# Kernel tuning notes

Measured on AMD Instinct MI355X. Metric: run time of the kernel, lower is better.

## Reference

```python
import jax, jax.numpy as jnp
import numpy as np

DIM = 4096
N_HEADS = 32
HEAD_DIM = 128
N_KV_HEADS = 8
KV_REPEATS = N_HEADS // N_KV_HEADS
SLIDING_WINDOW = 4096
SEQLEN = 2048
SCALE = HEAD_DIM ** -0.5
NEG = -1e9


def calculate_rope(x, cos, sin):
    # x: [S, H, D]; cos/sin: [S, D//2] applied to interleaved channel pairs
    x1, x2 = x[..., ::2], x[..., 1::2]
    c, s = cos[:, None, :], sin[:, None, :]
    r1 = x1 * c - x2 * s
    r2 = x1 * s + x2 * c
    return jnp.stack([r1, r2], axis=-1).reshape(x.shape)


def setup_inputs() -> dict:
    key = jax.random.key(0)
    ks = jax.random.split(key, 8)
    x = jax.random.normal(ks[0], (SEQLEN, DIM), dtype=jnp.float32)
    # rotary tables
    inv_freq = 1.0 / (10000.0 ** (np.arange(0, HEAD_DIM, 2, dtype=np.float32) / HEAD_DIM))
    t = np.arange(SEQLEN, dtype=np.float32)
    freqs = np.outer(t, inv_freq)  # [S, D/2]
    cos_freq = jnp.asarray(np.cos(freqs), dtype=jnp.float32)
    sin_freq = jnp.asarray(np.sin(freqs), dtype=jnp.float32)
    positions = jnp.arange(SEQLEN, dtype=jnp.int32)
    # causal sliding-window additive mask
    i = np.arange(SEQLEN)[:, None]
    j = np.arange(SEQLEN)[None, :]
    allow = (j <= i) & (j > i - SLIDING_WINDOW)
    mask = jnp.asarray(np.where(allow, 0.0, NEG), dtype=jnp.float32)
    cache_k = jnp.zeros((SLIDING_WINDOW, N_KV_HEADS, HEAD_DIM), dtype=jnp.float32)
    cache_v = jnp.zeros((SLIDING_WINDOW, N_KV_HEADS, HEAD_DIM), dtype=jnp.float32)
    # eqx.nn.Linear weights have shape (out_features, in_features)
    sd = DIM ** -0.5
    wq = jax.random.normal(ks[1], (N_HEADS * HEAD_DIM, DIM), dtype=jnp.float32) * sd
    wk = jax.random.normal(ks[2], (N_KV_HEADS * HEAD_DIM, DIM), dtype=jnp.float32) * sd
    wv = jax.random.normal(ks[3], (N_KV_HEADS * HEAD_DIM, DIM), dtype=jnp.float32) * sd
    wo = jax.random.normal(ks[4], (DIM, N_HEADS * HEAD_DIM), dtype=jnp.float32) * (N_HEADS * HEAD_DIM) ** -0.5
    return {"x": x, "cos_freq": cos_freq, "sin_freq": sin_freq, "positions": positions,
            "mask": mask, "cache_k": cache_k, "cache_v": cache_v,
            "wq": wq, "wk": wk, "wv": wv, "wo": wo}


def reference(x, cos_freq, sin_freq, positions, mask, cache_k, cache_v, wq, wk, wv, wo):
    seqlen = x.shape[0]
    xq = (x @ wq.T).reshape(seqlen, N_HEADS, HEAD_DIM)
    xk = (x @ wk.T).reshape(seqlen, N_KV_HEADS, HEAD_DIM)
    xv = (x @ wv.T).reshape(seqlen, N_KV_HEADS, HEAD_DIM)
    xq = calculate_rope(xq, cos_freq, sin_freq)
    xk = calculate_rope(xk, cos_freq, sin_freq)
    # prefill branch (positions.shape[0] > 1): scatter into sliding-window cache
    cache_k = cache_k.at[positions, :, :].set(xk[positions, :, :], mode='drop')
    cache_v = cache_v.at[positions, :, :].set(xv[positions, :, :], mode='drop')
    # GQA repeat kv heads
    k = jnp.repeat(xk, KV_REPEATS, axis=1)  # [S, H, D]
    v = jnp.repeat(xv, KV_REPEATS, axis=1)
    # scores: [H, Sq, Sk]
    scores = jnp.einsum('qhd,khd->hqk', xq, k) * SCALE
    scores = scores + mask[None, ...]
    probs = jax.nn.softmax(scores.astype(jnp.float32), axis=-1).astype(xq.dtype)
    out = jnp.einsum('hqk,khd->qhd', probs, v).reshape(seqlen, N_HEADS * HEAD_DIM)
    output = out @ wo.T
    return output, cache_k, cache_v
```

## Files before the change

kernel.cpp:

```cpp
#include <hip/hip_runtime.h>

typedef unsigned short ushort_t;
typedef unsigned int uint_t;
typedef __attribute__((ext_vector_type(8))) short bf16x8;
typedef __attribute__((ext_vector_type(4))) float floatx4;
typedef __attribute__((ext_vector_type(16))) float floatx16;

#define SEQ 2048
#define DIM 4096
#define NH 32
#define NKV 8
#define HD 128
#define KVDIM 1024
#define QKVN 6144

__device__ __forceinline__ ushort_t f2b(float f) {
  union { float f; uint_t u; } x; x.f = f;
  uint_t u = x.u;
  u += 0x7fffu + ((u >> 16) & 1u);
  return (ushort_t)(u >> 16);
}

#define GLOAD_LDS(g, l) \
  __builtin_amdgcn_global_load_lds((const __attribute__((address_space(1))) void*)(g), \
                                   (__attribute__((address_space(3))) void*)(l), 16, 0, 0)

__global__ __launch_bounds__(256) void cvt_all(const float* __restrict__ x,
                                               const float* __restrict__ wq,
                                               const float* __restrict__ wk,
                                               const float* __restrict__ wv,
                                               const float* __restrict__ wo,
                                               ushort_t* __restrict__ xb,
                                               ushort_t* __restrict__ wqkvb,
                                               ushort_t* __restrict__ wob) {
  int b = blockIdx.x;
  const float* src; ushort_t* dst; int i;
  if (b < 4096)       { src = x;  dst = xb;               i = b * 256 + threadIdx.x; }
  else if (b < 12288) { src = wq; dst = wqkvb;            i = (b - 4096) * 256 + threadIdx.x; }
  else if (b < 14336) { src = wk; dst = wqkvb + 16777216; i = (b - 12288) * 256 + threadIdx.x; }
  else if (b < 16384) { src = wv; dst = wqkvb + 20971520; i = (b - 14336) * 256 + threadIdx.x; }
  else                { src = wo; dst = wob;              i = (b - 16384) * 256 + threadIdx.x; }
  const float4* s = (const float4*)src;
  float4 a = s[2 * i], c = s[2 * i + 1];
  union { ushort_t u[8]; uint4 v; } o;
  o.u[0] = f2b(a.x); o.u[1] = f2b(a.y); o.u[2] = f2b(a.z); o.u[3] = f2b(a.w);
  o.u[4] = f2b(c.x); o.u[5] = f2b(c.y); o.u[6] = f2b(c.z); o.u[7] = f2b(c.w);
  ((uint4*)dst)[i] = o.v;
}

__global__ __launch_bounds__(256) void gemm128(const ushort_t* __restrict__ A,
                                               const ushort_t* __restrict__ B,
                                               float* __restrict__ C,
                                               int N, int K) {
  __shared__ __attribute__((aligned(16))) ushort_t lds_a[128 * 64];
  __shared__ __attribute__((aligned(16))) ushort_t lds_b[128 * 64];
  int tid = threadIdx.x;
  int lane = tid & 63;
  int w = tid >> 6;
  int m0 = blockIdx.y * 128, n0 = blockIdx.x * 128;
  int wm = (w >> 1) * 64, wn = (w & 1) * 64;
  int r32 = lane & 31, half = lane >> 5;

  const ushort_t* Ag[4]; const ushort_t* Bg[4];
  ushort_t* la[4]; ushort_t* lb[4];
#pragma unroll
  for (int e = 0; e < 4; ++e) {
    int l = e * 256 + tid;
    int row = l >> 3;
    int cg = (l & 7) ^ (row & 7);
    Ag[e] = A + (size_t)(m0 + row) * K + cg * 8;
    Bg[e] = B + (size_t)(n0 + row) * K + cg * 8;
    la[e] = &lds_a[(size_t)(e * 256 + (tid & ~63)) * 8];
    lb[e] = &lds_b[(size_t)(e * 256 + (tid & ~63)) * 8];
  }

  floatx16 acc[2][2] = {};
  for (int k0 = 0; k0 < K; k0 += 64) {
#pragma unroll
    for (int e = 0; e < 4; ++e) GLOAD_LDS(Ag[e] + k0, la[e]);
#pragma unroll
    for (int e = 0; e < 4; ++e) GLOAD_LDS(Bg[e] + k0, lb[e]);
    __syncthreads();
#pragma unroll
    for (int ks = 0; ks < 4; ++ks) {
      int c = ks * 2 + half;
      bf16x8 af[2], bfr[2];
#pragma unroll
      for (int mt = 0; mt < 2; ++mt) {
        int row = wm + mt * 32 + r32;
        af[mt] = *(const bf16x8*)&lds_a[row * 64 + (c ^ (row & 7)) * 8];
      }
#pragma unroll
      for (int nt = 0; nt < 2; ++nt) {
        int row = wn + nt * 32 + r32;
        bfr[nt] = *(const bf16x8*)&lds_b[row * 64 + (c ^ (row & 7)) * 8];
      }
#pragma unroll
      for (int mt = 0; mt < 2; ++mt)
#pragma unroll
        for (int nt = 0; nt < 2; ++nt)
          acc[mt][nt] = __builtin_amdgcn_mfma_f32_32x32x16_bf16(af[mt], bfr[nt], acc[mt][nt], 0, 0, 0);
    }
    __syncthreads();
  }
#pragma unroll
  for (int mt = 0; mt < 2; ++mt)
#pragma unroll
    for (int nt = 0; nt < 2; ++nt)
#pragma unroll
      for (int reg = 0; reg < 16; ++reg) {
        int rrow = (reg & 3) + 8 * (reg >> 2) + 4 * half;
        C[(size_t)(m0 + wm + mt * 32 + rrow) * N + n0 + wn + nt * 32 + r32] = acc[mt][nt][reg];
      }
}

__global__ __launch_bounds__(256) void posteps(const float* __restrict__ qkv,
                                               const float* __restrict__ cosf,
                                               const float* __restrict__ sinf,
                                               ushort_t* __restrict__ qb,
                                               ushort_t* __restrict__ kb,
                                               float* __restrict__ out) {
  int b = blockIdx.x;
  if (b < 16384) {
    const float QS = 1.4426950408889634f * 0.08838834764831845f;
    int idx = b * 256 + threadIdx.x;
    int pos = idx >> 11;
    int p = idx & 2047;
    int h = p >> 6, i = p & 63;
    size_t sb = (size_t)pos * QKVN + h * HD + 2 * i;
    float x1 = qkv[sb], x2 = qkv[sb + 1];
    float c = cosf[pos * 64 + i], s = sinf[pos * 64 + i];
    float r1 = (x1 * c - x2 * s) * QS;
    float r2 = (x1 * s + x2 * c) * QS;
    size_t db = (size_t)pos * DIM + h * HD + 2 * i;
    ((uint_t*)qb)[db >> 1] = (uint_t)f2b(r1) | ((uint_t)f2b(r2) << 16);
  } else if (b < 20480) {
    int idx = (b - 16384) * 256 + threadIdx.x;
    int pos = idx >> 9;
    int p = idx & 511;
    int kvh = p >> 6, i = p & 63;
    size_t sb = (size_t)pos * QKVN + DIM + kvh * HD + 2 * i;
    float x1 = qkv[sb], x2 = qkv[sb + 1];
    float c = cosf[pos * 64 + i], s = sinf[pos * 64 + i];
    float r1 = x1 * c - x2 * s;
    float r2 = x1 * s + x2 * c;
    size_t db = (size_t)pos * KVDIM + kvh * HD + 2 * i;
    ((uint_t*)kb)[db >> 1] = (uint_t)f2b(r1) | ((uint_t)f2b(r2) << 16);
    float2 cv; cv.x = r1; cv.y = r2;
    ((float2*)(out + 8388608))[db >> 1] = cv;
  } else {
    int i = (b - 20480) * 256 + threadIdx.x;
    float4 z = {0.f, 0.f, 0.f, 0.f};
    ((float4*)(out + 10485760))[i] = z;
    ((float4*)(out + 14680064))[i] = z;
  }
}

__global__ __launch_bounds__(256) void vt_cache(const float* __restrict__ qkv,
                                                ushort_t* __restrict__ vtb,
                                                float* __restrict__ cache_v) {
  __shared__ float tile[64][65];
  int pos0 = blockIdx.x * 64, c0 = blockIdx.y * 64;
  int t = threadIdx.x;
  int pr = t >> 4, cq = (t & 15) * 4;
#pragma unroll
  for (int rr = 0; rr < 4; ++rr) {
    int prow = pr + rr * 16;
    float4 v = *(const float4*)(qkv + (size_t)(pos0 + prow) * QKVN + DIM + KVDIM + c0 + cq);
    *(float4*)(cache_v + (size_t)(pos0 + prow) * KVDIM + c0 + cq) = v;
    tile[prow][cq] = v.x; tile[prow][cq + 1] = v.y;
    tile[prow][cq + 2] = v.z; tile[prow][cq + 3] = v.w;
  }
  __syncthreads();
  int dc = t >> 2, pg = (t & 3) * 16;
  int kvh = c0 >> 7, dl = (c0 & 127) + dc;
  union { ushort_t u[16]; uint4 q[2]; } o;
#pragma unroll
  for (int e = 0; e < 16; ++e) o.u[e] = f2b(tile[pg + e][dc]);
  uint4* dst = (uint4*)(vtb + (size_t)kvh * (HD * SEQ) + (size_t)dl * SEQ + pos0 + pg);
  dst[0] = o.q[0]; dst[1] = o.q[1];
}

__global__ __launch_bounds__(256) void attn(const ushort_t* __restrict__ Q,
                                            const ushort_t* __restrict__ Kb,
                                            const ushort_t* __restrict__ Vt,
                                            ushort_t* __restrict__ O) {
  int h = blockIdx.y;
  int kvh = h >> 2;
  int tid = threadIdx.x;
  int w = tid >> 6, lane = tid & 63;
  int row = lane & 15, quad = lane >> 4;

  __shared__ __attribute__((aligned(16))) ushort_t lds_k[64][136];
  __shared__ __attribute__((aligned(16))) ushort_t lds_vt[128][72];
  __shared__ __attribute__((aligned(16))) float p_lds[4][16][68];

  int kr = tid >> 2, kc = (tid & 3) * 32;
  int vd = tid >> 1, vj = (tid & 1) * 32;
  const ushort_t* kg = Kb + (size_t)kr * KVDIM + kvh * HD + kc;
  const ushort_t* vg = Vt + (size_t)kvh * (HD * SEQ) + (size_t)vd * SEQ + vj;

#pragma unroll 1
  for (int ph = 0; ph < 2; ++ph) {
    int qb = ph ? (31 - blockIdx.x) : blockIdx.x;
    int q0 = qb * 64 + w * 16;

    bf16x8 qf[4];
    const ushort_t* qp = Q + (size_t)(q0 + row) * DIM + h * HD + quad * 8;
#pragma unroll
    for (int ks = 0; ks < 4; ++ks) qf[ks] = *(const bf16x8*)(qp + ks * 32);

    floatx4 o_acc[8] = {};
    float l_r[4] = {0.f, 0.f, 0.f, 0.f};

    for (int kt = 0; kt <= qb; ++kt) {
      int kv0 = kt * 64;
#pragma unroll
      for (int e = 0; e < 4; ++e)
        *(bf16x8*)&lds_k[kr][kc + e * 8] = *(const bf16x8*)(kg + (size_t)kv0 * KVDIM + e * 8);
#pragma unroll
      for (int e = 0; e < 4; ++e)
        *(bf16x8*)&lds_vt[vd][vj + e * 8] = *(const bf16x8*)(vg + kv0 + e * 8);
      __syncthreads();

      floatx4 s[4] = {};
#pragma unroll
      for (int j2 = 0; j2 < 4; ++j2)
#pragma unroll
        for (int ks = 0; ks < 4; ++ks) {
          bf16x8 kfrag = *(const bf16x8*)&lds_k[j2 * 16 + row][ks * 32 + quad * 8];
          s[j2] = __builtin_amdgcn_mfma_f32_16x16x32_bf16(qf[ks], kfrag, s[j2], 0, 0, 0);
        }

      bool diag = (kt == qb);
      float pv[4][4];
#pragma unroll
      for (int j2 = 0; j2 < 4; ++j2)
#pragma unroll
        for (int r = 0; r < 4; ++r) {
          float v = s[j2][r];
          if (diag) {
            int j_g = kv0 + j2 * 16 + row;
            int i_g = q0 + quad * 4 + r;
            v += (j_g <= i_g) ? 0.f : -1e9f;
          }
          float p = exp2f(v);
          pv[j2][r] = p;
          l_r[r] += p;
        }
#pragma unroll
      for (int j2 = 0; j2 < 4; ++j2)
#pragma unroll
        for (int r = 0; r < 4; ++r) p_lds[w][quad * 4 + r][j2 * 16 + row] = pv[j2][r];
      bf16x8 pf[2];
#pragma unroll
      for (int kb2 = 0; kb2 < 2; ++kb2) {
        float4 pa = *(const float4*)&p_lds[w][row][kb2 * 32 + quad * 8];
        float4 pb = *(const float4*)&p_lds[w][row][kb2 * 32 + quad * 8 + 4];
        union { bf16x8 v; ushort_t u[8]; } pu;
        pu.u[0] = f2b(pa.x); pu.u[1] = f2b(pa.y); pu.u[2] = f2b(pa.z); pu.u[3] = f2b(pa.w);
        pu.u[4] = f2b(pb.x); pu.u[5] = f2b(pb.y); pu.u[6] = f2b(pb.z); pu.u[7] = f2b(pb.w);
        pf[kb2] = pu.v;
      }
#pragma unroll
      for (int db = 0; db < 8; ++db)
#pragma unroll
        for (int kb2 = 0; kb2 < 2; ++kb2) {
          bf16x8 vfrag = *(const bf16x8*)&lds_vt[db * 16 + row][kb2 * 32 + quad * 8];
          o_acc[db] = __builtin_amdgcn_mfma_f32_16x16x32_bf16(pf[kb2], vfrag, o_acc[db], 0, 0, 0);
        }
      __syncthreads();
    }

#pragma unroll
    for (int off = 1; off < 16; off <<= 1)
#pragma unroll
      for (int r = 0; r < 4; ++r) l_r[r] += __shfl_xor(l_r[r], off, 64);
    float inv[4];
#pragma unroll
    for (int r = 0; r < 4; ++r) inv[r] = 1.0f / l_r[r];
#pragma unroll
    for (int db = 0; db < 8; ++db)
#pragma unroll
      for (int r = 0; r < 4; ++r)
        O[(size_t)(q0 + quad * 4 + r) * DIM + h * HD + db * 16 + row] = f2b(o_acc[db][r] * inv[r]);
  }
}

extern "C" void kernel_launch(void* const* d_in, const int* in_sizes, int n_in,
                              void* d_out, int out_size, void* d_ws, size_t ws_size,
                              hipStream_t stream) {
  const float* x    = (const float*)d_in[0];
  const float* cosf = (const float*)d_in[1];
  const float* sinf = (const float*)d_in[2];
  const float* wq = (const float*)d_in[7];
  const float* wk = (const float*)d_in[8];
  const float* wv = (const float*)d_in[9];
  const float* wo = (const float*)d_in[10];
  float* out = (float*)d_out;
  float* cache_v_out = out + 12582912;

  char* ws = (char*)d_ws;
  ushort_t* xb     = (ushort_t*)(ws + 0);
  ushort_t* wqkvb  = (ushort_t*)(ws + 16777216);
  ushort_t* wob    = (ushort_t*)(ws + 67108864);
  float*    qkv32  = (float*)(ws + 100663296);
  ushort_t* qbuf   = (ushort_t*)(ws + 150994944);
  ushort_t* kbuf   = (ushort_t*)(ws + 167772160);
  ushort_t* vtb    = (ushort_t*)(ws + 171966464);
  ushort_t* attnb  = (ushort_t*)(ws + 176160768);

  cvt_all<<<24576, 256, 0, stream>>>(x, wq, wk, wv, wo, xb, wqkvb, wob);
  gemm128<<<dim3(48, 16), 256, 0, stream>>>(xb, wqkvb, qkv32, QKVN, DIM);
  posteps<<<22528, 256, 0, stream>>>(qkv32, cosf, sinf, qbuf, kbuf, out);
  vt_cache<<<dim3(32, 16), 256, 0, stream>>>(qkv32, vtb, cache_v_out);
  attn<<<dim3(16, 32), 256, 0, stream>>>(qbuf, kbuf, vtb, attnb);
  gemm128<<<dim3(32, 16), 256, 0, stream>>>(attnb, wob, out, DIM, DIM);
}
```

Measured before the change: 565.4 us.

## Replace GEMM with 8-wave 128x256 double-buffered pipelined kernel

Replaces the single-stage 128x128 GEMM with a 512-thread, 128x256-tile kernel that double-buffers LDS and interleaves global-to-LDS loads with MFMA quadrants, using explicit vmcnt waits and barriers. It also remaps workgroups across XCDs for L2 locality, switches to 16x16x32 MFMA, and raises MFMA priority with setprio. The aim is to hide memory latency and improve reuse in both projection GEMMs, at the cost of hand-tuned waitcnt logic that must be exactly right and higher LDS/register use.

```diff
diff --git a/kernel.cpp b/kernel.cpp
--- a/kernel.cpp
+++ b/kernel.cpp
@@ -24,6 +24,9 @@
 #define GLOAD_LDS(g, l) \
   __builtin_amdgcn_global_load_lds((const __attribute__((address_space(1))) void*)(g), \
                                    (__attribute__((address_space(3))) void*)(l), 16, 0, 0)
+
+#define BARX() asm volatile("s_barrier" ::: "memory")
+#define WAIT_VM(n) asm volatile("s_waitcnt vmcnt(" #n ")" ::: "memory")
 
 __global__ __launch_bounds__(256) void cvt_all(const float* __restrict__ x,
                                                const float* __restrict__ wq,
@@ -48,70 +51,116 @@
   ((uint4*)dst)[i] = o.v;
 }
 
-__global__ __launch_bounds__(256) void gemm128(const ushort_t* __restrict__ A,
-                                               const ushort_t* __restrict__ B,
-                                               float* __restrict__ C,
-                                               int N, int K) {
-  __shared__ __attribute__((aligned(16))) ushort_t lds_a[128 * 64];
-  __shared__ __attribute__((aligned(16))) ushort_t lds_b[128 * 64];
+__global__ __launch_bounds__(512, 2) void gemm8p(const ushort_t* __restrict__ A,
+                                                 const ushort_t* __restrict__ B,
+                                                 float* __restrict__ C,
+                                                 int N, int K) {
+  __shared__ __attribute__((aligned(16))) ushort_t sA[2][8192];
+  __shared__ __attribute__((aligned(16))) ushort_t sB[2][16384];
+
   int tid = threadIdx.x;
   int lane = tid & 63;
   int w = tid >> 6;
-  int m0 = blockIdx.y * 128, n0 = blockIdx.x * 128;
-  int wm = (w >> 1) * 64, wn = (w & 1) * 64;
-  int r32 = lane & 31, half = lane >> 5;
-
-  const ushort_t* Ag[4]; const ushort_t* Bg[4];
-  ushort_t* la[4]; ushort_t* lb[4];
-#pragma unroll
-  for (int e = 0; e < 4; ++e) {
-    int l = e * 256 + tid;
-    int row = l >> 3;
-    int cg = (l & 7) ^ (row & 7);
-    Ag[e] = A + (size_t)(m0 + row) * K + cg * 8;
-    Bg[e] = B + (size_t)(n0 + row) * K + cg * 8;
-    la[e] = &lds_a[(size_t)(e * 256 + (tid & ~63)) * 8];
-    lb[e] = &lds_b[(size_t)(e * 256 + (tid & ~63)) * 8];
+  int wm = w >> 2, wn = w & 3;
+  int l15 = lane & 15, l4 = lane >> 4;
+  int e7 = l15 & 7;
+  int co0 = ((l4 ^ e7) << 3);
+  int co1 = co0 ^ 32;
+
+  int nwg = (int)gridDim.x;
+  int ntn = N >> 8;
+  int lin = ((int)blockIdx.x & 7) * (nwg >> 3) + ((int)blockIdx.x >> 3);
+  int m0 = (lin / ntn) << 7;
+  int n0 = (lin % ntn) << 8;
+
+  int nkt = K >> 6;
+  int niter = nkt >> 1;
+
+  int r0 = tid >> 3;
+  int c0 = ((tid & 7) ^ (r0 & 7)) << 3;
+  const ushort_t* sa0 = A + (size_t)(m0 + r0) * K + c0;
+  const ushort_t* sb0 = B + (size_t)(n0 + r0) * K + c0;
+  const ushort_t* sb1 = sb0 + (size_t)128 * K;
+  int d0 = (tid & ~63) << 3;
+  size_t ek = (size_t)64 * K;
+
+#define STA(kk, s)  do { GLOAD_LDS(sa0 + (kk), &sA[s][d0]); \
+                         GLOAD_LDS(sa0 + ek + (kk), &sA[s][d0 + 4096]); } while (0)
+#define STB0(kk, s) do { GLOAD_LDS(sb0 + (kk), &sB[s][d0]); \
+                         GLOAD_LDS(sb0 + ek + (kk), &sB[s][d0 + 4096]); } while (0)
+#define STB1(kk, s) do { GLOAD_LDS(sb1 + (kk), &sB[s][8192 + d0]); \
+                         GLOAD_LDS(sb1 + ek + (kk), &sB[s][8192 + d0 + 4096]); } while (0)
+
+  floatx4 acc[4][4] = {};
+  bf16x8 a[4][2], b[4][2];
+
+#define RDA2(s, RG) do { const ushort_t* pa = &sA[s][(wm * 64 + l15) * 64]; \
+  _Pragma("unroll") for (int rg = 0; rg < 2; ++rg) { \
+    a[RG + rg][0] = *(const bf16x8*)&pa[(RG + rg) * 1024 + co0]; \
+    a[RG + rg][1] = *(const bf16x8*)&pa[(RG + rg) * 1024 + co1]; } } while (0)
+#define RDB2(s, CG) do { const ushort_t* pb = &sB[s][(wn * 64 + l15) * 64]; \
+  _Pragma("unroll") for (int cg = 0; cg < 2; ++cg) { \
+    b[CG + cg][0] = *(const bf16x8*)&pb[(CG + cg) * 1024 + co0]; \
+    b[CG + cg][1] = *(const bf16x8*)&pb[(CG + cg) * 1024 + co1]; } } while (0)
+
+#define QUAD(RG, CG) do { __builtin_amdgcn_s_setprio(1); \
+  _Pragma("unroll") for (int rg = 0; rg < 2; ++rg) \
+  _Pragma("unroll") for (int cg = 0; cg < 2; ++cg) \
+  _Pragma("unroll") for (int ks = 0; ks < 2; ++ks) \
+    acc[RG + rg][CG + cg] = __builtin_amdgcn_mfma_f32_16x16x32_bf16( \
+        a[RG + rg][ks], b[CG + cg][ks], acc[RG + rg][CG + cg], 0, 0, 0); \
+  __builtin_amdgcn_s_setprio(0); } while (0)
+
+  STA(0, 0); STB0(0, 0); STB1(0, 0);
+  STA(64, 1); STB0(64, 1);
+  WAIT_VM(4);
+  BARX();
+
+#pragma unroll 1
+  for (int i = 0; i < niter; ++i) {
+    int k1 = (2 * i + 1) << 6;
+    int t2 = 2 * i + 2; if (t2 > nkt - 1) t2 = nkt - 1;
+    int t3 = 2 * i + 3; if (t3 > nkt - 1) t3 = nkt - 1;
+    int k2 = t2 << 6, k3 = t3 << 6;
+
+    RDA2(0, 0); RDB2(0, 0); RDA2(0, 2);
+    STB1(k1, 1);
+    BARX(); QUAD(0, 0); BARX();
+    RDB2(0, 2);
+    STA(k2, 0);
+    BARX(); QUAD(0, 2); BARX();
+    STB0(k2, 0);
+    BARX(); QUAD(2, 0); BARX();
+    STB1(k2, 0);
+    WAIT_VM(6);
+    BARX(); QUAD(2, 2); BARX();
+
+    RDA2(1, 0); RDB2(1, 0); RDA2(1, 2);
+    BARX(); QUAD(0, 0); BARX();
+    RDB2(1, 2);
+    STA(k3, 1);
+    BARX(); QUAD(0, 2); BARX();
+    STB0(k3, 1);
+    BARX(); QUAD(2, 0); BARX();
+    WAIT_VM(4);
+    BARX(); QUAD(2, 2); BARX();
   }
 
-  floatx16 acc[2][2] = {};
-  for (int k0 = 0; k0 < K; k0 += 64) {
-#pragma unroll
-    for (int e = 0; e < 4; ++e) GLOAD_LDS(Ag[e] + k0, la[e]);
-#pragma unroll
-    for (int e = 0; e < 4; ++e) GLOAD_LDS(Bg[e] + k0, lb[e]);
-    __syncthreads();
-#pragma unroll
-    for (int ks = 0; ks < 4; ++ks) {
-      int c = ks * 2 + half;
-      bf16x8 af[2], bfr[2];
-#pragma unroll
-      for (int mt = 0; mt < 2; ++mt) {
-        int row = wm + mt * 32 + r32;
-        af[mt] = *(const bf16x8*)&lds_a[row * 64 + (c ^ (row & 7)) * 8];
-      }
-#pragma unroll
-      for (int nt = 0; nt < 2; ++nt) {
-        int row = wn + nt * 32 + r32;
-        bfr[nt] = *(const bf16x8*)&lds_b[row * 64 + (c ^ (row & 7)) * 8];
-      }
-#pragma unroll
-      for (int mt = 0; mt < 2; ++mt)
-#pragma unroll
-        for (int nt = 0; nt < 2; ++nt)
-          acc[mt][nt] = __builtin_amdgcn_mfma_f32_32x32x16_bf16(af[mt], bfr[nt], acc[mt][nt], 0, 0, 0);
+#pragma unroll
+  for (int rg = 0; rg < 4; ++rg)
+#pragma unroll
+    for (int cg = 0; cg < 4; ++cg) {
+      float* cp = C + (size_t)(m0 + wm * 64 + rg * 16 + l4 * 4) * N
+                    + (n0 + wn * 64 + cg * 16 + l15);
+#pragma unroll
+      for (int r = 0; r < 4; ++r) cp[(size_t)r * N] = acc[rg][cg][r];
     }
-    __syncthreads();
-  }
-#pragma unroll
-  for (int mt = 0; mt < 2; ++mt)
-#pragma unroll
-    for (int nt = 0; nt < 2; ++nt)
-#pragma unroll
-      for (int reg = 0; reg < 16; ++reg) {
-        int rrow = (reg & 3) + 8 * (reg >> 2) + 4 * half;
-        C[(size_t)(m0 + wm + mt * 32 + rrow) * N + n0 + wn + nt * 32 + r32] = acc[mt][nt][reg];
-      }
+#undef STA
+#undef STB0
+#undef STB1
+#undef RDA2
+#undef RDB2
+#undef QUAD
 }
 
 __global__ __launch_bounds__(256) void posteps(const float* __restrict__ qkv,
@@ -311,9 +360,9 @@
   ushort_t* attnb  = (ushort_t*)(ws + 176160768);
 
   cvt_all<<<24576, 256, 0, stream>>>(x, wq, wk, wv, wo, xb, wqkvb, wob);
-  gemm128<<<dim3(48, 16), 256, 0, stream>>>(xb, wqkvb, qkv32, QKVN, DIM);
+  gemm8p<<<384, 512, 0, stream>>>(xb, wqkvb, qkv32, QKVN, DIM);
   posteps<<<22528, 256, 0, stream>>>(qkv32, cosf, sinf, qbuf, kbuf, out);
   vt_cache<<<dim3(32, 16), 256, 0, stream>>>(qkv32, vtb, cache_v_out);
   attn<<<dim3(16, 32), 256, 0, stream>>>(qbuf, kbuf, vtb, attnb);
-  gemm128<<<dim3(32, 16), 256, 0, stream>>>(attnb, wob, out, DIM, DIM);
-}
+  gemm8p<<<256, 512, 0, stream>>>(attnb, wob, out, DIM, DIM);
+}
```

After: 594.6 us. 1.05x slower.
